# Optimization experiments

Hardware: AMD Instinct MI355X
Metric: run time of the kernel (lower is better)

Reference implementation:

```python
import jax, jax.numpy as jnp
import numpy as np

B, C, P, HP, WP = 128, 3, 196, 16, 16  # batch, channels, patches, patch h, patch w
E = 768  # embedding size; patches_pixel_count = C*HP*WP = 768


def setup_inputs() -> dict:
    key = jax.random.key(0)
    ks = jax.random.split(key, 9)
    return {
        "inputs": jax.random.normal(ks[0], (B, C, P, HP, WP), dtype=jnp.float32),
        "W1": jax.random.normal(ks[1], (C * HP * WP, 32), dtype=jnp.float32) * 0.02,
        "b1": jax.random.normal(ks[2], (32,), dtype=jnp.float32) * 0.02,
        "W2": jax.random.normal(ks[3], (32, 64), dtype=jnp.float32) * 0.02,
        "b2": jax.random.normal(ks[4], (64,), dtype=jnp.float32) * 0.02,
        "W3": jax.random.normal(ks[5], (64, E), dtype=jnp.float32) * 0.02,
        "b3": jax.random.normal(ks[6], (E,), dtype=jnp.float32) * 0.02,
        "cls_token": jax.random.normal(ks[7], (1, E), dtype=jnp.float32) * 0.02,
        "pos_enc": jax.random.normal(ks[8], (P + 1, E), dtype=jnp.float32) * 0.02,
    }


def reference(inputs, W1, b1, W2, b2, W3, b3, cls_token, pos_enc):
    b, c, p, hp, wp = inputs.shape
    # per-patch slab is [C, hp, wp] flattened in (C, h, w) order -> [B, P, C*hp*wp]
    x = jnp.transpose(inputs, (0, 2, 1, 3, 4)).reshape(b, p, c * hp * wp)
    x = x @ W1 + b1          # [B, P, 32]
    x = x @ W2 + b2          # [B, P, 64]
    x = x @ W3 + b3          # [B, P, E]
    cls = jnp.broadcast_to(cls_token[None], (b, 1, cls_token.shape[-1]))
    x = jnp.concatenate([cls, x], axis=1)  # [B, P+1, E]
    return x + pos_enc[None]               # broadcast add of position encodings
```

## Files before the change

### kernel.cpp

```cpp
#include <hip/hip_runtime.h>


#define BATCH 128
#define CH    3
#define NP    196
#define PIX   256
#define K1    768
#define NH    64
#define EMB   768

typedef __bf16 bf16x8 __attribute__((ext_vector_type(8)));
typedef float  f32x4  __attribute__((ext_vector_type(4)));

#define W12T_OFF 0
#define W3T_OFF  98304
#define B12_OFF  196608
#define POSB_OFF 196864

__global__ __launch_bounds__(256) void patchembed_prep1(
    const float* __restrict__ W1, const float* __restrict__ W2,
    const float* __restrict__ b1, const float* __restrict__ b2,
    __bf16* __restrict__ w12t, float* __restrict__ b12)
{
    const int i = blockIdx.x * 256 + threadIdx.x;
    if (i < NH * K1) {
        const int n = i / K1, k = i - n * K1;
        float s = 0.f;
        #pragma unroll
        for (int j = 0; j < 32; ++j) s += W1[k * 32 + j] * W2[j * NH + n];
        w12t[i] = (__bf16)s;
    } else if (i < NH * K1 + NH) {
        const int n = i - NH * K1;
        float s = b2[n];
        #pragma unroll
        for (int j = 0; j < 32; ++j) s += b1[j] * W2[j * NH + n];
        b12[n] = s;
    }
}

__global__ __launch_bounds__(256) void patchembed_prep2(
    const float* __restrict__ W3, const float* __restrict__ b3,
    const float* __restrict__ cls, const float* __restrict__ pos,
    const float* __restrict__ b12,
    __bf16* __restrict__ w3t, float* __restrict__ posb, float* __restrict__ out)
{
    const int i = blockIdx.x * 256 + threadIdx.x;
    const int T1 = EMB * NH;
    const int T2 = T1 + 197 * EMB;
    const int T3 = T2 + BATCH * EMB;
    if (i < T1) {
        const int col = i >> 6, kk = i & 63;
        w3t[i] = (__bf16)W3[kk * EMB + col];
    } else if (i < T2) {
        const int j = i - T1;
        const int r = j / EMB, c = j - r * EMB;
        float v = pos[j];
        if (r == 0) {
            v += cls[c];
        } else {
            float s = b3[c];
            #pragma unroll
            for (int n = 0; n < NH; ++n) s += b12[n] * W3[n * EMB + c];
            v += s;
        }
        posb[j] = v;
    } else if (i < T3) {
        const int j = i - T2;
        const int b = j / EMB, c = j - b * EMB;
        out[b * (197 * EMB) + c] = cls[c] + pos[c];
    }
}

__global__ __launch_bounds__(256, 4) void patchembed_main(
    const float* __restrict__ X,
    const __bf16* __restrict__ w12t,
    const __bf16* __restrict__ w3t,
    const float*  __restrict__ posb,
    float* __restrict__ out)
{
    __shared__ __align__(16) float h1p[4][16][68];

    const int tid  = threadIdx.x;
    const int wv   = tid >> 6;
    const int lane = tid & 63;
    const int l15  = lane & 15;
    const int q    = lane >> 4;
    const int r0   = blockIdx.x * 16;

    int obase[4], pbase[4];
    #pragma unroll
    for (int r = 0; r < 4; ++r) {
        const int row = r0 + q * 4 + r;
        const int b = row / NP, p = row - b * NP;
        obase[r] = (b * 197 + p + 1) * EMB;
        pbase[r] = (p + 1) * EMB;
    }

    {
        const int xrow = r0 + l15;
        const int b = xrow / NP, p = xrow - b * NP;
        const float* xb = X + ((b * CH) * NP + p) * PIX;
        const int kb0 = wv * 6;

        float4 u[6], v[6];
        #pragma unroll
        for (int t = 0; t < 6; ++t) {
            const int kb = kb0 + t;
            const float* ptr = xb + (kb >> 3) * (NP * PIX) + (kb & 7) * 32 + q * 8;
            u[t] = *(const float4*)ptr;
            v[t] = *(const float4*)(ptr + 4);
        }

        f32x4 acc0 = {0.f, 0.f, 0.f, 0.f};
        f32x4 acc1 = acc0, acc2 = acc0, acc3 = acc0;
        #pragma unroll
        for (int t = 0; t < 6; ++t) {
            const int kb = kb0 + t;
            bf16x8 a;
            a[0] = (__bf16)u[t].x; a[1] = (__bf16)u[t].y;
            a[2] = (__bf16)u[t].z; a[3] = (__bf16)u[t].w;
            a[4] = (__bf16)v[t].x; a[5] = (__bf16)v[t].y;
            a[6] = (__bf16)v[t].z; a[7] = (__bf16)v[t].w;
            const __bf16* wb = w12t + kb * 32 + q * 8;
            bf16x8 f0 = *(const bf16x8*)(wb + l15 * K1);
            bf16x8 f1 = *(const bf16x8*)(wb + (16 + l15) * K1);
            bf16x8 f2 = *(const bf16x8*)(wb + (32 + l15) * K1);
            bf16x8 f3 = *(const bf16x8*)(wb + (48 + l15) * K1);
            acc0 = __builtin_amdgcn_mfma_f32_16x16x32_bf16(a, f0, acc0, 0, 0, 0);
            acc1 = __builtin_amdgcn_mfma_f32_16x16x32_bf16(a, f1, acc1, 0, 0, 0);
            acc2 = __builtin_amdgcn_mfma_f32_16x16x32_bf16(a, f2, acc2, 0, 0, 0);
            acc3 = __builtin_amdgcn_mfma_f32_16x16x32_bf16(a, f3, acc3, 0, 0, 0);
        }
        #pragma unroll
        for (int r = 0; r < 4; ++r) {
            h1p[wv][q * 4 + r][l15]      = acc0[r];
            h1p[wv][q * 4 + r][16 + l15] = acc1[r];
            h1p[wv][q * 4 + r][32 + l15] = acc2[r];
            h1p[wv][q * 4 + r][48 + l15] = acc3[r];
        }
    }
    __syncthreads();

    const int c0l = wv * 192 + l15;
    bf16x8 F0[2][3], F1[2][3];
    float  pb[2][3][4];

#define LOADG(buf, g)                                                         \
    {                                                                         \
        _Pragma("unroll")                                                     \
        for (int t = 0; t < 3; ++t) {                                         \
            const int col = c0l + ((g) * 3 + t) * 16;                         \
            const __bf16* wr = w3t + col * NH;                                \
            F0[buf][t] = *(const bf16x8*)(wr + q * 8);                        \
            F1[buf][t] = *(const bf16x8*)(wr + 32 + q * 8);                   \
            _Pragma("unroll")                                                 \
            for (int r = 0; r < 4; ++r) pb[buf][t][r] = posb[pbase[r] + col]; \
        }                                                                     \
    }

    bf16x8 a0, a1;

#define COMPG(buf, g)                                                         \
    {                                                                         \
        _Pragma("unroll")                                                     \
        for (int t = 0; t < 3; ++t) {                                         \
            const int col = c0l + ((g) * 3 + t) * 16;                         \
            f32x4 z = {0.f, 0.f, 0.f, 0.f};                                   \
            f32x4 c = __builtin_amdgcn_mfma_f32_16x16x32_bf16(a0, F0[buf][t], z, 0, 0, 0); \
            c = __builtin_amdgcn_mfma_f32_16x16x32_bf16(a1, F1[buf][t], c, 0, 0, 0);       \
            _Pragma("unroll")                                                 \
            for (int r = 0; r < 4; ++r) out[obase[r] + col] = c[r] + pb[buf][t][r];        \
        }                                                                     \
    }

    LOADG(0, 0)

    {
        f32x4 s0a = {0.f, 0.f, 0.f, 0.f};
        f32x4 s0b = s0a, s1a = s0a, s1b = s0a;
        #pragma unroll
        for (int w = 0; w < 4; ++w) {
            const float* hp = &h1p[w][l15][0];
            s0a += *(const f32x4*)(hp + q * 8);
            s0b += *(const f32x4*)(hp + q * 8 + 4);
            s1a += *(const f32x4*)(hp + 32 + q * 8);
            s1b += *(const f32x4*)(hp + 32 + q * 8 + 4);
        }
        #pragma unroll
        for (int j = 0; j < 4; ++j) {
            a0[j] = (__bf16)s0a[j]; a0[4 + j] = (__bf16)s0b[j];
            a1[j] = (__bf16)s1a[j]; a1[4 + j] = (__bf16)s1b[j];
        }
    }

    LOADG(1, 1)
    COMPG(0, 0)
    LOADG(0, 2)
    COMPG(1, 1)
    LOADG(1, 3)
    COMPG(0, 2)
    COMPG(1, 3)

#undef LOADG
#undef COMPG
}

extern "C" void kernel_launch(void* const* d_in, const int* in_sizes, int n_in,
                              void* d_out, int out_size, void* d_ws, size_t ws_size,
                              hipStream_t stream)
{
    const float* X   = (const float*)d_in[0];
    const float* W1  = (const float*)d_in[1];
    const float* b1  = (const float*)d_in[2];
    const float* W2  = (const float*)d_in[3];
    const float* b2  = (const float*)d_in[4];
    const float* W3  = (const float*)d_in[5];
    const float* b3  = (const float*)d_in[6];
    const float* cls = (const float*)d_in[7];
    const float* pos = (const float*)d_in[8];
    float* out = (float*)d_out;

    char* ws = (char*)d_ws;
    __bf16* w12t = (__bf16*)(ws + W12T_OFF);
    __bf16* w3t  = (__bf16*)(ws + W3T_OFF);
    float*  b12  = (float*)(ws + B12_OFF);
    float*  posb = (float*)(ws + POSB_OFF);

    patchembed_prep1<<<193, 256, 0, stream>>>(W1, W2, b1, b2, w12t, b12);
    patchembed_prep2<<<1167, 256, 0, stream>>>(W3, b3, cls, pos, b12, w3t, posb, out);
    patchembed_main<<<1568, 256, 0, stream>>>(X, w12t, w3t, posb, out);
}
```

Measured before the change: 199.0 us.

## Split fused patch-embed kernel into two stages via bf16 intermediate buffer

Splits the fused main kernel into two kernels. The first computes the 64-wide hidden activations and writes them to a bf16 workspace buffer. The second reads them and computes the 768-wide output, with each wave handling a 16-row by 96-column tile, which doubles the block count for the output stage. The aim is to decouple the input-read phase from the output-write phase and raise parallelism and occupancy, at the cost of an extra launch and an intermediate round-trip through global memory. The software double-buffered loads in the old output phase are dropped.

```diff
diff --git a/kernel.cpp b/kernel.cpp
--- a/kernel.cpp
+++ b/kernel.cpp
@@ -8,6 +8,7 @@
 #define K1    768
 #define NH    64
 #define EMB   768
+#define NROW  (BATCH * NP)
 
 typedef __bf16 bf16x8 __attribute__((ext_vector_type(8)));
 typedef float  f32x4  __attribute__((ext_vector_type(4)));
@@ -16,6 +17,7 @@
 #define W3T_OFF  98304
 #define B12_OFF  196608
 #define POSB_OFF 196864
+#define H_OFF    802048
 
 __global__ __launch_bounds__(256) void patchembed_prep1(
     const float* __restrict__ W1, const float* __restrict__ W2,
@@ -71,12 +73,10 @@
     }
 }
 
-__global__ __launch_bounds__(256, 4) void patchembed_main(
+__global__ __launch_bounds__(256) void patchembed_s1(
     const float* __restrict__ X,
     const __bf16* __restrict__ w12t,
-    const __bf16* __restrict__ w3t,
-    const float*  __restrict__ posb,
-    float* __restrict__ out)
+    __bf16* __restrict__ H)
 {
     __shared__ __align__(16) float h1p[4][16][68];
 
@@ -87,40 +87,25 @@
     const int q    = lane >> 4;
     const int r0   = blockIdx.x * 16;
 
-    int obase[4], pbase[4];
-    #pragma unroll
-    for (int r = 0; r < 4; ++r) {
-        const int row = r0 + q * 4 + r;
-        const int b = row / NP, p = row - b * NP;
-        obase[r] = (b * 197 + p + 1) * EMB;
-        pbase[r] = (p + 1) * EMB;
-    }
-
     {
         const int xrow = r0 + l15;
         const int b = xrow / NP, p = xrow - b * NP;
         const float* xb = X + ((b * CH) * NP + p) * PIX;
         const int kb0 = wv * 6;
 
-        float4 u[6], v[6];
+        f32x4 acc0 = {0.f, 0.f, 0.f, 0.f};
+        f32x4 acc1 = acc0, acc2 = acc0, acc3 = acc0;
         #pragma unroll
         for (int t = 0; t < 6; ++t) {
             const int kb = kb0 + t;
             const float* ptr = xb + (kb >> 3) * (NP * PIX) + (kb & 7) * 32 + q * 8;
-            u[t] = *(const float4*)ptr;
-            v[t] = *(const float4*)(ptr + 4);
-        }
-
-        f32x4 acc0 = {0.f, 0.f, 0.f, 0.f};
-        f32x4 acc1 = acc0, acc2 = acc0, acc3 = acc0;
-        #pragma unroll
-        for (int t = 0; t < 6; ++t) {
-            const int kb = kb0 + t;
+            float4 u = *(const float4*)ptr;
+            float4 v = *(const float4*)(ptr + 4);
             bf16x8 a;
-            a[0] = (__bf16)u[t].x; a[1] = (__bf16)u[t].y;
-            a[2] = (__bf16)u[t].z; a[3] = (__bf16)u[t].w;
-            a[4] = (__bf16)v[t].x; a[5] = (__bf16)v[t].y;
-            a[6] = (__bf16)v[t].z; a[7] = (__bf16)v[t].w;
+            a[0] = (__bf16)u.x; a[1] = (__bf16)u.y;
+            a[2] = (__bf16)u.z; a[3] = (__bf16)u.w;
+            a[4] = (__bf16)v.x; a[5] = (__bf16)v.y;
+            a[6] = (__bf16)v.z; a[7] = (__bf16)v.w;
             const __bf16* wb = w12t + kb * 32 + q * 8;
             bf16x8 f0 = *(const bf16x8*)(wb + l15 * K1);
             bf16x8 f1 = *(const bf16x8*)(wb + (16 + l15) * K1);
@@ -141,41 +126,7 @@
     }
     __syncthreads();
 
-    const int c0l = wv * 192 + l15;
-    bf16x8 F0[2][3], F1[2][3];
-    float  pb[2][3][4];
-
-#define LOADG(buf, g)                                                         \
-    {                                                                         \
-        _Pragma("unroll")                                                     \
-        for (int t = 0; t < 3; ++t) {                                         \
-            const int col = c0l + ((g) * 3 + t) * 16;                         \
-            const __bf16* wr = w3t + col * NH;                                \
-            F0[buf][t] = *(const bf16x8*)(wr + q * 8);                        \
-            F1[buf][t] = *(const bf16x8*)(wr + 32 + q * 8);                   \
-            _Pragma("unroll")                                                 \
-            for (int r = 0; r < 4; ++r) pb[buf][t][r] = posb[pbase[r] + col]; \
-        }                                                                     \
-    }
-
-    bf16x8 a0, a1;
-
-#define COMPG(buf, g)                                                         \
-    {                                                                         \
-        _Pragma("unroll")                                                     \
-        for (int t = 0; t < 3; ++t) {                                         \
-            const int col = c0l + ((g) * 3 + t) * 16;                         \
-            f32x4 z = {0.f, 0.f, 0.f, 0.f};                                   \
-            f32x4 c = __builtin_amdgcn_mfma_f32_16x16x32_bf16(a0, F0[buf][t], z, 0, 0, 0); \
-            c = __builtin_amdgcn_mfma_f32_16x16x32_bf16(a1, F1[buf][t], c, 0, 0, 0);       \
-            _Pragma("unroll")                                                 \
-            for (int r = 0; r < 4; ++r) out[obase[r] + col] = c[r] + pb[buf][t][r];        \
-        }                                                                     \
-    }
-
-    LOADG(0, 0)
-
-    {
+    if (wv == 0) {
         f32x4 s0a = {0.f, 0.f, 0.f, 0.f};
         f32x4 s0b = s0a, s1a = s0a, s1b = s0a;
         #pragma unroll
@@ -186,23 +137,67 @@
             s1a += *(const f32x4*)(hp + 32 + q * 8);
             s1b += *(const f32x4*)(hp + 32 + q * 8 + 4);
         }
+        bf16x8 a0, a1;
         #pragma unroll
         for (int j = 0; j < 4; ++j) {
             a0[j] = (__bf16)s0a[j]; a0[4 + j] = (__bf16)s0b[j];
             a1[j] = (__bf16)s1a[j]; a1[4 + j] = (__bf16)s1b[j];
         }
-    }
-
-    LOADG(1, 1)
-    COMPG(0, 0)
-    LOADG(0, 2)
-    COMPG(1, 1)
-    LOADG(1, 3)
-    COMPG(0, 2)
-    COMPG(1, 3)
-
-#undef LOADG
-#undef COMPG
+        __bf16* hr = H + (r0 + l15) * NH;
+        *(bf16x8*)(hr + q * 8)      = a0;
+        *(bf16x8*)(hr + 32 + q * 8) = a1;
+    }
+}
+
+__global__ __launch_bounds__(256) void patchembed_s2(
+    const __bf16* __restrict__ H,
+    const __bf16* __restrict__ w3t,
+    const float*  __restrict__ posb,
+    float* __restrict__ out)
+{
+    const int tid  = threadIdx.x;
+    const int wv   = tid >> 6;
+    const int lane = tid & 63;
+    const int l15  = lane & 15;
+    const int q    = lane >> 4;
+
+    const int wave_id = blockIdx.x * 4 + wv;
+    const int rt = wave_id >> 3;
+    const int cs = wave_id & 7;
+    const int r0 = rt * 16;
+
+    const __bf16* hr = H + (r0 + l15) * NH;
+    bf16x8 a0 = *(const bf16x8*)(hr + q * 8);
+    bf16x8 a1 = *(const bf16x8*)(hr + 32 + q * 8);
+
+    int obase[4], pbase[4];
+    #pragma unroll
+    for (int r = 0; r < 4; ++r) {
+        const int row = r0 + q * 4 + r;
+        const int b = row / NP, p = row - b * NP;
+        obase[r] = (b * 197 + p + 1) * EMB;
+        pbase[r] = (p + 1) * EMB;
+    }
+
+    const int c0 = cs * 96 + l15;
+    #pragma unroll
+    for (int t = 0; t < 6; ++t) {
+        const int col = c0 + t * 16;
+        const __bf16* wr = w3t + col * NH;
+        bf16x8 f0 = *(const bf16x8*)(wr + q * 8);
+        bf16x8 f1 = *(const bf16x8*)(wr + 32 + q * 8);
+        float pb0 = posb[pbase[0] + col];
+        float pb1 = posb[pbase[1] + col];
+        float pb2 = posb[pbase[2] + col];
+        float pb3 = posb[pbase[3] + col];
+        f32x4 z = {0.f, 0.f, 0.f, 0.f};
+        f32x4 c = __builtin_amdgcn_mfma_f32_16x16x32_bf16(a0, f0, z, 0, 0, 0);
+        c       = __builtin_amdgcn_mfma_f32_16x16x32_bf16(a1, f1, c, 0, 0, 0);
+        out[obase[0] + col] = c[0] + pb0;
+        out[obase[1] + col] = c[1] + pb1;
+        out[obase[2] + col] = c[2] + pb2;
+        out[obase[3] + col] = c[3] + pb3;
+    }
 }
 
 extern "C" void kernel_launch(void* const* d_in, const int* in_sizes, int n_in,
@@ -225,8 +220,10 @@
     __bf16* w3t  = (__bf16*)(ws + W3T_OFF);
     float*  b12  = (float*)(ws + B12_OFF);
     float*  posb = (float*)(ws + POSB_OFF);
+    __bf16* H    = (__bf16*)(ws + H_OFF);
 
     patchembed_prep1<<<193, 256, 0, stream>>>(W1, W2, b1, b2, w12t, b12);
     patchembed_prep2<<<1167, 256, 0, stream>>>(W3, b3, cls, pos, b12, w3t, posb, out);
-    patchembed_main<<<1568, 256, 0, stream>>>(X, w12t, w3t, posb, out);
-}
+    patchembed_s1<<<NROW / 16, 256, 0, stream>>>(X, w12t, H);
+    patchembed_s2<<<NROW / 16 * 2, 256, 0, stream>>>(H, w3t, posb, out);
+}
```

Result: faster. 189.5 us (-4.8%).
